# Optimization experiments

Hardware: AMD Instinct MI355X
Metric: run time of the kernel (lower is better)

## Reference

```python
import jax, jax.numpy as jnp
import numpy as np

N = 16_777_216  # number of samples


def setup_inputs() -> dict:
    key = jax.random.key(0)
    k1, k2 = jax.random.split(key)
    confs = jax.random.uniform(k1, (N,), dtype=jnp.float32)  # confidences in [0,1)
    # binary correctness indicators (float, as accs[in_bin].float() in torch)
    accs = (jax.random.uniform(k2, (N,), dtype=jnp.float32) < 0.8).astype(jnp.float32)
    return {"confs": confs, "accs": accs, "n_bins": 20}


def reference(confs, accs, n_bins):
    # boundaries = linspace(0.5, 1, n_bins+1); bin j holds boundaries[j] < c <= boundaries[j+1]
    boundaries = jnp.linspace(0.5, 1.0, n_bins + 1, dtype=jnp.float32)
    # searchsorted(side='left') returns first i with boundaries[i] >= c, so bin = i - 1
    bin_idx = jnp.searchsorted(boundaries, confs, side='left') - 1
    valid = (bin_idx >= 0) & (bin_idx < n_bins)  # c > 0.5 and c <= 1.0
    seg = jnp.where(valid, bin_idx, n_bins)  # invalid samples go to a discard bin

    counts = jax.ops.segment_sum(valid.astype(jnp.float32), seg, num_segments=n_bins + 1)[:n_bins]
    conf_sum = jax.ops.segment_sum(confs, seg, num_segments=n_bins + 1)[:n_bins]
    acc_sum = jax.ops.segment_sum(accs, seg, num_segments=n_bins + 1)[:n_bins]

    n_total = confs.shape[0]
    prop_in_bin = counts / n_total
    denom = jnp.maximum(counts, 1.0)  # guard empty bins
    avg_conf = conf_sum / denom
    avg_acc = acc_sum / denom
    ece = jnp.sum(jnp.where(counts > 0, jnp.abs(avg_conf - avg_acc) * prop_in_bin, 0.0))
    return ece.reshape(1)
```

## Files before the change

### kernel.cpp

```cpp
#include <hip/hip_runtime.h>
#include <hip/hip_bf16.h>

#define NBINS 20
#define NSLOT 21
#define TPB 256

__global__ __launch_bounds__(TPB) void ece_accum(
        const float4* __restrict__ confs,
        const float4* __restrict__ accs,
        int n8,
        float* __restrict__ partials,
        int nb) {
    __shared__ float s[NSLOT * TPB];
    __shared__ float red[NBINS][TPB / 64];
    const int t = threadIdx.x;
#pragma unroll
    for (int k = 0; k < NSLOT; ++k) s[k * TPB + t] = 0.0f;
    __syncthreads();

    const int tid = blockIdx.x * TPB + t;
    const int stride = gridDim.x * TPB;

#pragma unroll 2
    for (int i = tid; i < n8; i += stride) {
        float4 c4a = confs[2 * i];
        float4 c4b = confs[2 * i + 1];
        float4 a4a = accs[2 * i];
        float4 a4b = accs[2 * i + 1];
#pragma unroll
        for (int j = 0; j < 8; ++j) {
            float c, a;
            switch (j) {
                case 0: c = c4a.x; a = a4a.x; break;
                case 1: c = c4a.y; a = a4a.y; break;
                case 2: c = c4a.z; a = a4a.z; break;
                case 3: c = c4a.w; a = a4a.w; break;
                case 4: c = c4b.x; a = a4b.x; break;
                case 5: c = c4b.y; a = a4b.y; break;
                case 6: c = c4b.z; a = a4b.z; break;
                default: c = c4b.w; a = a4b.w; break;
            }
            float ft = __builtin_ceilf((c - 0.5f) * 40.0f);
            unsigned int bin = (unsigned int)((int)ft - 1);
            bin = bin < (unsigned int)NBINS ? bin : (unsigned int)NBINS;
            s[bin * TPB + t] += c - a;
        }
    }
    __syncthreads();

    const int wave = t >> 6, lane = t & 63;
#pragma unroll
    for (int b = 0; b < NBINS; ++b) {
        float v = s[b * TPB + t];
#pragma unroll
        for (int m = 32; m >= 1; m >>= 1) v += __shfl_xor(v, m, 64);
        if (lane == 0) red[b][wave] = v;
    }
    __syncthreads();
    if (t < NBINS) {
        float sum = red[t][0] + red[t][1] + red[t][2] + red[t][3];
        partials[t * nb + blockIdx.x] = sum;
    }
}

__global__ __launch_bounds__(512) void ece_final(
        const float* __restrict__ partials,
        float* __restrict__ out,
        float inv_n, int nb) {
    float s[NBINS];
#pragma unroll
    for (int b = 0; b < NBINS; ++b) s[b] = 0.0f;

    const int tid = threadIdx.x;
    const int nb4 = nb >> 2;
#pragma unroll
    for (int b = 0; b < NBINS; ++b) {
        const float4* pb = (const float4*)(partials + b * nb);
        for (int k = tid; k < nb4; k += blockDim.x) {
            float4 v = pb[k];
            s[b] += (v.x + v.y) + (v.z + v.w);
        }
    }
#pragma unroll
    for (int b = 0; b < NBINS; ++b) {
#pragma unroll
        for (int m = 32; m >= 1; m >>= 1)
            s[b] += __shfl_xor(s[b], m, 64);
    }

    __shared__ float red[NBINS][8];
    const int wave = tid >> 6;
    const int lane = tid & 63;
    if (lane == 0) {
#pragma unroll
        for (int b = 0; b < NBINS; ++b) red[b][wave] = s[b];
    }
    __syncthreads();

    if (tid == 0) {
        float ece = 0.0f;
#pragma unroll
        for (int b = 0; b < NBINS; ++b) {
            float t = 0.0f;
#pragma unroll
            for (int w = 0; w < 8; ++w) t += red[b][w];
            ece += fabsf(t);
        }
        out[0] = ece * inv_n;
    }
}

extern "C" void kernel_launch(void* const* d_in, const int* in_sizes, int n_in,
                              void* d_out, int out_size, void* d_ws, size_t ws_size,
                              hipStream_t stream) {
    const float* confs = (const float*)d_in[0];
    const float* accs = (const float*)d_in[1];
    const int n = in_sizes[0];
    const int n8 = n / 8;

    int nb = 1792;
    int ws_cap = (int)(ws_size / (NBINS * sizeof(float)));
    ws_cap &= ~3;
    if (nb > ws_cap) nb = ws_cap;
    if (nb < 4) nb = 4;

    float* partials = (float*)d_ws;

    ece_accum<<<nb, TPB, 0, stream>>>((const float4*)confs, (const float4*)accs,
                                      n8, partials, nb);
    ece_final<<<1, 512, 0, stream>>>(partials, (float*)d_out, 1.0f / (float)n, nb);
}
```

Before: 42.06 us.

## Software-prefetch next iteration loads and shrink LDS histogram to boost occupancy

New measurement: 42.50 us. About the same (+1.1%).

```diff
diff --git a/kernel.cpp b/kernel.cpp
--- a/kernel.cpp
+++ b/kernel.cpp
@@ -2,63 +2,85 @@
 #include <hip/hip_bf16.h>
 
 #define NBINS 20
-#define NSLOT 21
 #define TPB 256
 
-__global__ __launch_bounds__(TPB) void ece_accum(
+__global__ __launch_bounds__(TPB, 8) void ece_accum(
         const float4* __restrict__ confs,
         const float4* __restrict__ accs,
         int n8,
         float* __restrict__ partials,
         int nb) {
-    __shared__ float s[NSLOT * TPB];
-    __shared__ float red[NBINS][TPB / 64];
+    __shared__ float s[NBINS * TPB];
     const int t = threadIdx.x;
 #pragma unroll
-    for (int k = 0; k < NSLOT; ++k) s[k * TPB + t] = 0.0f;
+    for (int k = 0; k < NBINS; ++k) s[k * TPB + t] = 0.0f;
     __syncthreads();
 
-    const int tid = blockIdx.x * TPB + t;
     const int stride = gridDim.x * TPB;
+    int i = blockIdx.x * TPB + t;
 
-#pragma unroll 2
-    for (int i = tid; i < n8; i += stride) {
-        float4 c4a = confs[2 * i];
-        float4 c4b = confs[2 * i + 1];
-        float4 a4a = accs[2 * i];
-        float4 a4b = accs[2 * i + 1];
+    float4 c0, c1, a0, a1;
+    bool have = (i < n8);
+    if (have) {
+        c0 = confs[2 * i];
+        c1 = confs[2 * i + 1];
+        a0 = accs[2 * i];
+        a1 = accs[2 * i + 1];
+    }
+
+    while (have) {
+        const int inext = i + stride;
+        const bool hnext = (inext < n8);
+        float4 nc0, nc1, na0, na1;
+        if (hnext) {
+            nc0 = confs[2 * inext];
+            nc1 = confs[2 * inext + 1];
+            na0 = accs[2 * inext];
+            na1 = accs[2 * inext + 1];
+        }
+
 #pragma unroll
         for (int j = 0; j < 8; ++j) {
             float c, a;
             switch (j) {
-                case 0: c = c4a.x; a = a4a.x; break;
-                case 1: c = c4a.y; a = a4a.y; break;
-                case 2: c = c4a.z; a = a4a.z; break;
-                case 3: c = c4a.w; a = a4a.w; break;
-                case 4: c = c4b.x; a = a4b.x; break;
-                case 5: c = c4b.y; a = a4b.y; break;
-                case 6: c = c4b.z; a = a4b.z; break;
-                default: c = c4b.w; a = a4b.w; break;
+                case 0: c = c0.x; a = a0.x; break;
+                case 1: c = c0.y; a = a0.y; break;
+                case 2: c = c0.z; a = a0.z; break;
+                case 3: c = c0.w; a = a0.w; break;
+                case 4: c = c1.x; a = a1.x; break;
+                case 5: c = c1.y; a = a1.y; break;
+                case 6: c = c1.z; a = a1.z; break;
+                default: c = c1.w; a = a1.w; break;
             }
             float ft = __builtin_ceilf((c - 0.5f) * 40.0f);
             unsigned int bin = (unsigned int)((int)ft - 1);
-            bin = bin < (unsigned int)NBINS ? bin : (unsigned int)NBINS;
-            s[bin * TPB + t] += c - a;
+            if (bin < (unsigned int)NBINS)
+                s[bin * TPB + t] += c - a;
         }
+
+        i = inext;
+        have = hnext;
+        c0 = nc0; c1 = nc1; a0 = na0; a1 = na1;
     }
     __syncthreads();
 
-    const int wave = t >> 6, lane = t & 63;
+    float v[NBINS];
+#pragma unroll
+    for (int b = 0; b < NBINS; ++b) v[b] = s[b * TPB + t];
 #pragma unroll
     for (int b = 0; b < NBINS; ++b) {
-        float v = s[b * TPB + t];
 #pragma unroll
-        for (int m = 32; m >= 1; m >>= 1) v += __shfl_xor(v, m, 64);
-        if (lane == 0) red[b][wave] = v;
+        for (int m = 32; m >= 1; m >>= 1) v[b] += __shfl_xor(v[b], m, 64);
+    }
+    __syncthreads();
+    const int wave = t >> 6, lane = t & 63;
+    if (lane == 0) {
+#pragma unroll
+        for (int b = 0; b < NBINS; ++b) s[b * 4 + wave] = v[b];
     }
     __syncthreads();
     if (t < NBINS) {
-        float sum = red[t][0] + red[t][1] + red[t][2] + red[t][3];
+        float sum = s[t * 4 + 0] + s[t * 4 + 1] + s[t * 4 + 2] + s[t * 4 + 3];
         partials[t * nb + blockIdx.x] = sum;
     }
 }
@@ -101,10 +123,10 @@
         float ece = 0.0f;
 #pragma unroll
         for (int b = 0; b < NBINS; ++b) {
-            float t = 0.0f;
+            float tt = 0.0f;
 #pragma unroll
-            for (int w = 0; w < 8; ++w) t += red[b][w];
-            ece += fabsf(t);
+            for (int w = 0; w < 8; ++w) tt += red[b][w];
+            ece += fabsf(tt);
         }
         out[0] = ece * inv_n;
     }
@@ -118,7 +140,7 @@
     const int n = in_sizes[0];
     const int n8 = n / 8;
 
-    int nb = 1792;
+    int nb = 2048;
     int ws_cap = (int)(ws_size / (NBINS * sizeof(float)));
     ws_cap &= ~3;
     if (nb > ws_cap) nb = ws_cap;
```
